# Performance work log

Hardware: AMD Instinct MI355X
Metric: run time of the kernel (lower is better)

The kernel has to match this reference:

```python
import jax, jax.numpy as jnp
import numpy as np

B, S, D, H, DH = 2, 2048, 1024, 16, 64
GLOBAL_RATIO = 0.1
LN_EPS = 1e-5


def setup_inputs() -> dict:
    key = jax.random.key(0)
    ks = jax.random.split(key, 8)
    w = lambda k, shape: jax.random.normal(k, shape, jnp.float32) * 0.02
    return {
        'x': jax.random.normal(ks[0], (B, S, D), jnp.float32),
        'Wq': w(ks[1], (D, H * DH)),
        'Wk': w(ks[2], (D, H * DH)),
        'Wv': w(ks[3], (D, H * DH)),
        'Wo': w(ks[4], (H * DH, D)),
        'bo': jnp.zeros((D,), jnp.float32),
        'ln_gamma': jnp.ones((DH,), jnp.float32),
        'ln_beta': jnp.zeros((DH,), jnp.float32),
        'Wg': w(ks[5], (2 * DH, DH)),
        'bg': jnp.zeros((DH,), jnp.float32),
    }


def _layernorm(x, gamma, beta):
    mu = jnp.mean(x, axis=-1, keepdims=True)
    var = jnp.mean(jnp.square(x - mu), axis=-1, keepdims=True)
    return (x - mu) * jax.lax.rsqrt(var + LN_EPS) * gamma + beta


def reference(x, Wq, Wk, Wv, Wo, bo, ln_gamma, ln_beta, Wg, bg):
    b, s, _ = x.shape
    # projections -> [b, h, n, d]
    split = lambda t: t.reshape(b, s, H, DH).transpose(0, 2, 1, 3)
    q = split(x @ Wq)
    k = split(x @ Wk)
    v = split(x @ Wv)
    scale = DH ** -0.5

    # local (full) attention: manual QK^T / softmax / AV
    scores = jnp.einsum('bhnd,bhmd->bhnm', q, k) * scale  # [b,h,s,s]
    attn = jax.nn.softmax(scores, axis=-1)
    local_out = jnp.einsum('bhnm,bhmd->bhnd', attn, v)

    # cross-segment fusion: top-k keys by norm per (b, h)
    num_global = max(1, int(s * GLOBAL_RATIO))
    key_norms = jnp.linalg.norm(k, axis=-1)  # [b,h,s]
    _, top_idx = jax.lax.top_k(key_norms, num_global)  # [b,h,g]
    idx = top_idx[..., None]  # [b,h,g,1]
    global_k = jnp.take_along_axis(k, idx, axis=2)  # [b,h,g,d]
    global_v = jnp.take_along_axis(v, idx, axis=2)
    g_scores = jnp.einsum('bhnd,bhgd->bhng', q, global_k) * scale
    g_attn = jax.nn.softmax(g_scores, axis=-1)
    global_out = jnp.einsum('bhng,bhgd->bhnd', g_attn, global_v)
    global_out = _layernorm(global_out, ln_gamma, ln_beta)

    # learned gate over [local, global]
    cat = jnp.concatenate([local_out, global_out], axis=-1)  # [b,h,s,2d]
    gate = jax.nn.sigmoid(cat @ Wg + bg)
    fused = gate * local_out + (1.0 - gate) * global_out

    out = fused.transpose(0, 2, 1, 3).reshape(b, s, H * DH)  # b h n d -> b n (h d)
    return out @ Wo + bo
```

## Files before the change

kernel.cpp:

```cpp
#include <hip/hip_runtime.h>


constexpr int SEQ    = 2048;
constexpr int DMODEL = 1024;
constexpr int NH     = 16;
constexpr int DHEAD  = 64;
constexpr int BHT    = 32;
constexpr int NG     = 204;
constexpr int NGPAD  = 256;
constexpr float LNEPS = 1e-5f;

typedef __attribute__((ext_vector_type(8))) short short8;
typedef __attribute__((ext_vector_type(4))) short short4v;
typedef __attribute__((ext_vector_type(4))) float f32x4;

__device__ __forceinline__ unsigned short f2bf(float f) {
    unsigned int u = __float_as_uint(f);
    u += 0x7FFFu + ((u >> 16) & 1u);
    return (unsigned short)(u >> 16);
}
__device__ __forceinline__ float bf2f(unsigned short b) {
    return __uint_as_float(((unsigned int)b) << 16);
}

__global__ __launch_bounds__(256)
void prep_k(const float* __restrict__ x,
            const float* __restrict__ Wq, const float* __restrict__ Wv,
            const float* __restrict__ Wo, const float* __restrict__ Wk,
            const float* __restrict__ Wg,
            unsigned short* __restrict__ xh, unsigned short* __restrict__ xl,
            unsigned short* __restrict__ Wqt, unsigned short* __restrict__ Wvt,
            unsigned short* __restrict__ Wot, unsigned short* __restrict__ Wkh,
            unsigned short* __restrict__ Wkl, unsigned short* __restrict__ Wgt)
{
    const int bid = blockIdx.x;
    const int tid = threadIdx.x;

    if (bid < 2048) {
        int i = (bid * 256 + tid) << 3;
        short8 h, l;
#pragma unroll
        for (int j = 0; j < 8; ++j) {
            float v = x[i + j];
            unsigned short hb = f2bf(v);
            h[j] = (short)hb;
            l[j] = (short)f2bf(v - bf2f(hb));
        }
        *(short8*)(xh + i) = h;
        *(short8*)(xl + i) = l;
        return;
    }
    if (bid == 3072) {
#pragma unroll
        for (int i = 0; i < 32; ++i) {
            int o = tid * 32 + i;
            int dg = o >> 7, jj = o & 127;
            Wgt[o] = f2bf(Wg[jj * 64 + dg]);
        }
        return;
    }

    __shared__ float tile[64][68];
    const int sub = bid - 2048;
    const int which = sub >> 8;
    const int b = sub & 255;
    const int n0 = (b & 15) * 64, k0 = (b >> 4) * 64;
    const float* W = (which == 0) ? Wq : (which == 1) ? Wv : (which == 2) ? Wo : Wk;
    const int Kd = DMODEL, Nd = DMODEL;

#pragma unroll
    for (int p = 0; p < 4; ++p) {
        int c = tid + (p << 8);
        int r = c >> 4, c4 = (c & 15) << 2;
        *(float4*)&tile[r][c4] = *(const float4*)(W + (size_t)(k0 + r) * Nd + n0 + c4);
    }
    __syncthreads();
#pragma unroll
    for (int p = 0; p < 4; ++p) {
        int c = tid + (p << 8);
        int n = c >> 4, k4 = (c & 15) << 2;
        if (which < 3) {
            unsigned short* Wt = (which == 0) ? Wqt : (which == 1) ? Wvt : Wot;
            short4v o;
#pragma unroll
            for (int j = 0; j < 4; ++j) o[j] = (short)f2bf(tile[k4 + j][n]);
            *(short4v*)(Wt + (size_t)(n0 + n) * Kd + k0 + k4) = o;
        } else {
            short4v oh, ol;
#pragma unroll
            for (int j = 0; j < 4; ++j) {
                float v = tile[k4 + j][n];
                unsigned short hb = f2bf(v);
                oh[j] = (short)hb;
                ol[j] = (short)f2bf(v - bf2f(hb));
            }
            *(short4v*)(Wkh + (size_t)(n0 + n) * Kd + k0 + k4) = oh;
            *(short4v*)(Wkl + (size_t)(n0 + n) * Kd + k0 + k4) = ol;
        }
    }
}

__global__ __launch_bounds__(512)
void gemm_bf16_k(const unsigned short* __restrict__ A,
                 const unsigned short* __restrict__ Bt,
                 const float* __restrict__ bias,
                 void* __restrict__ outv, void* __restrict__ outv2,
                 unsigned short* __restrict__ vtout,
                 int M, int N, int K, int mode)
{
    __shared__ __align__(16) unsigned short As[128][72];
    __shared__ __align__(16) unsigned short Bs[128][72];
    const int tid = threadIdx.x;
    const int lane = tid & 63, wave = tid >> 6;
    const int quad = lane >> 4, ln = lane & 15;
    const int mh = (wave >> 2) << 6;
    const int nh = (wave & 3) << 5;
    const int m0 = blockIdx.y * 128, n0 = blockIdx.x * 128;

    f32x4 acc[4][2];
#pragma unroll
    for (int i = 0; i < 4; ++i)
#pragma unroll
        for (int j = 0; j < 2; ++j) acc[i][j] = (f32x4){0.f, 0.f, 0.f, 0.f};

    short8 areg[2], breg[2];
#pragma unroll
    for (int p = 0; p < 2; ++p) {
        int c = tid + (p << 9);
        int row = c >> 3, col8 = (c & 7) << 3;
        areg[p] = *(const short8*)(A + (size_t)(m0 + row) * K + col8);
        breg[p] = *(const short8*)(Bt + (size_t)(n0 + row) * K + col8);
    }

    for (int k0 = 0; k0 < K; k0 += 64) {
        __syncthreads();
#pragma unroll
        for (int p = 0; p < 2; ++p) {
            int c = tid + (p << 9);
            int row = c >> 3, col8 = (c & 7) << 3;
            *(short8*)&As[row][col8] = areg[p];
            *(short8*)&Bs[row][col8] = breg[p];
        }
        __syncthreads();
        if (k0 + 64 < K) {
#pragma unroll
            for (int p = 0; p < 2; ++p) {
                int c = tid + (p << 9);
                int row = c >> 3, col8 = (c & 7) << 3;
                areg[p] = *(const short8*)(A + (size_t)(m0 + row) * K + k0 + 64 + col8);
                breg[p] = *(const short8*)(Bt + (size_t)(n0 + row) * K + k0 + 64 + col8);
            }
        }
#pragma unroll
        for (int ch = 0; ch < 2; ++ch) {
            short8 af[4], bf[2];
#pragma unroll
            for (int mt = 0; mt < 4; ++mt)
                af[mt] = *(const short8*)&As[mh + mt * 16 + ln][ch * 32 + quad * 8];
#pragma unroll
            for (int nt = 0; nt < 2; ++nt)
                bf[nt] = *(const short8*)&Bs[nh + nt * 16 + ln][ch * 32 + quad * 8];
#pragma unroll
            for (int mt = 0; mt < 4; ++mt)
#pragma unroll
                for (int nt = 0; nt < 2; ++nt)
                    acc[mt][nt] = __builtin_amdgcn_mfma_f32_16x16x32_bf16(
                        af[mt], bf[nt], acc[mt][nt], 0, 0, 0);
        }
    }

    if (mode == 0) {
        float* out = (float*)outv;
#pragma unroll
        for (int mt = 0; mt < 4; ++mt)
#pragma unroll
            for (int nt = 0; nt < 2; ++nt)
#pragma unroll
                for (int r = 0; r < 4; ++r) {
                    int m = m0 + mh + mt * 16 + quad * 4 + r;
                    int n = n0 + nh + nt * 16 + ln;
                    out[(size_t)m * N + n] = acc[mt][nt][r] + bias[n];
                }
    } else {
#pragma unroll
        for (int mt = 0; mt < 4; ++mt)
#pragma unroll
            for (int nt = 0; nt < 2; ++nt) {
                int n = n0 + nh + nt * 16 + ln;
                int mb = m0 + mh + mt * 16 + quad * 4;
                int b = mb >> 11, s0 = mb & (SEQ - 1);
                int d = n & 63;
                if (n < DMODEL) {
                    int h = n >> 6;
                    unsigned short* qp_ =
                        (unsigned short*)outv + ((size_t)(b * NH + h) * SEQ + s0) * DHEAD + d;
#pragma unroll
                    for (int r = 0; r < 4; ++r)
                        qp_[(size_t)r * DHEAD] = f2bf(acc[mt][nt][r] * 0.125f);
                } else {
                    int h = (n >> 6) - NH;
                    unsigned short* vp_ =
                        (unsigned short*)outv2 + ((size_t)(b * NH + h) * SEQ + s0) * DHEAD + d;
                    short4v tv;
#pragma unroll
                    for (int r = 0; r < 4; ++r) {
                        unsigned short bv = f2bf(acc[mt][nt][r]);
                        vp_[(size_t)r * DHEAD] = bv;
                        tv[r] = (short)bv;
                    }
                    *(short4v*)(vtout + ((size_t)(b * NH + h) * DHEAD + d) * SEQ + s0) = tv;
                }
            }
    }
}

__global__ __launch_bounds__(512)
void gemm_kproj_mfma(const unsigned short* __restrict__ xh,
                     const unsigned short* __restrict__ xl,
                     const unsigned short* __restrict__ Wh,
                     const unsigned short* __restrict__ Wl,
                     unsigned short* __restrict__ kout,
                     float* __restrict__ norms2)
{
    __shared__ __align__(16) unsigned short Ah[64][72];
    __shared__ __align__(16) unsigned short Al[64][72];
    __shared__ __align__(16) unsigned short Bh[128][72];
    __shared__ __align__(16) unsigned short Bl[128][72];
    const int K = DMODEL;
    const int tid = threadIdx.x;
    const int lane = tid & 63, wave = tid >> 6;
    const int quad = lane >> 4, ln = lane & 15;
    const int mh = (wave >> 1) << 4;
    const int nh = (wave & 1) << 6;
    const int m0 = blockIdx.y * 64, n0 = blockIdx.x * 128;

    f32x4 acc[4];
#pragma unroll
    for (int j = 0; j < 4; ++j) acc[j] = (f32x4){0.f, 0.f, 0.f, 0.f};

    const int arow = tid >> 3, acol8 = (tid & 7) << 3;
    short8 ahreg, alreg, bhreg[2], blreg[2];
    {
        size_t ga = (size_t)(m0 + arow) * K + acol8;
        ahreg = *(const short8*)(xh + ga);
        alreg = *(const short8*)(xl + ga);
#pragma unroll
        for (int p = 0; p < 2; ++p) {
            int c = tid + (p << 9);
            int row = c >> 3, col8 = (c & 7) << 3;
            size_t gb = (size_t)(n0 + row) * K + col8;
            bhreg[p] = *(const short8*)(Wh + gb);
            blreg[p] = *(const short8*)(Wl + gb);
        }
    }

    for (int k0 = 0; k0 < K; k0 += 64) {
        __syncthreads();
        *(short8*)&Ah[arow][acol8] = ahreg;
        *(short8*)&Al[arow][acol8] = alreg;
#pragma unroll
        for (int p = 0; p < 2; ++p) {
            int c = tid + (p << 9);
            int row = c >> 3, col8 = (c & 7) << 3;
            *(short8*)&Bh[row][col8] = bhreg[p];
            *(short8*)&Bl[row][col8] = blreg[p];
        }
        __syncthreads();
        if (k0 + 64 < K) {
            size_t ga = (size_t)(m0 + arow) * K + k0 + 64 + acol8;
            ahreg = *(const short8*)(xh + ga);
            alreg = *(const short8*)(xl + ga);
#pragma unroll
            for (int p = 0; p < 2; ++p) {
                int c = tid + (p << 9);
                int row = c >> 3, col8 = (c & 7) << 3;
                size_t gb = (size_t)(n0 + row) * K + k0 + 64 + col8;
                bhreg[p] = *(const short8*)(Wh + gb);
                blreg[p] = *(const short8*)(Wl + gb);
            }
        }
#pragma unroll
        for (int ch = 0; ch < 2; ++ch) {
            short8 bh4[4], bl4[4];
#pragma unroll
            for (int nt = 0; nt < 4; ++nt) {
                bh4[nt] = *(const short8*)&Bh[nh + nt * 16 + ln][ch * 32 + quad * 8];
                bl4[nt] = *(const short8*)&Bl[nh + nt * 16 + ln][ch * 32 + quad * 8];
            }
            short8 ah = *(const short8*)&Ah[mh + ln][ch * 32 + quad * 8];
            short8 al = *(const short8*)&Al[mh + ln][ch * 32 + quad * 8];
#pragma unroll
            for (int nt = 0; nt < 4; ++nt) {
                acc[nt] = __builtin_amdgcn_mfma_f32_16x16x32_bf16(ah, bh4[nt], acc[nt], 0, 0, 0);
                acc[nt] = __builtin_amdgcn_mfma_f32_16x16x32_bf16(ah, bl4[nt], acc[nt], 0, 0, 0);
                acc[nt] = __builtin_amdgcn_mfma_f32_16x16x32_bf16(al, bh4[nt], acc[nt], 0, 0, 0);
            }
        }
    }

    const int h = (n0 + nh) >> 6;
#pragma unroll
    for (int r = 0; r < 4; ++r) {
        int m = m0 + mh + quad * 4 + r;
        int b = m >> 11, s = m & (SEQ - 1);
        size_t rowbase = ((size_t)(b * NH + h) * SEQ + s) * DHEAD;
#pragma unroll
        for (int nt = 0; nt < 4; ++nt)
            kout[rowbase + nt * 16 + ln] = f2bf(acc[nt][r]);
        float s2 = acc[0][r] * acc[0][r] + acc[1][r] * acc[1][r] +
                   acc[2][r] * acc[2][r] + acc[3][r] * acc[3][r];
#pragma unroll
        for (int off = 1; off <= 8; off <<= 1)
            s2 += __shfl_xor(s2, off);
        if (ln == 0)
            norms2[(size_t)(b * NH + h) * SEQ + s] = s2;
    }
}

__global__ __launch_bounds__(512)
void topk_gather_k(const float* __restrict__ norms2,
                   const unsigned short* __restrict__ k,
                   const unsigned short* __restrict__ v,
                   unsigned short* __restrict__ gk,
                   unsigned short* __restrict__ gvt)
{
    __shared__ unsigned long long keys[SEQ];
    __shared__ int tix[NGPAD];
    __shared__ __align__(16) unsigned short T[64][72];
    const int bh = blockIdx.x;
    const int tid = threadIdx.x;
    const float* nb = norms2 + (size_t)bh * SEQ;
    const size_t base = (size_t)bh * SEQ * DHEAD;

    for (int i = tid; i < SEQ; i += 512) {
        float nrm = sqrtf(nb[i]);
        keys[i] = ((unsigned long long)__float_as_uint(nrm) << 32) |
                  (unsigned int)(0xFFFFFFFFu - (unsigned int)i);
    }
    __syncthreads();
    for (int kk = 2; kk <= SEQ; kk <<= 1) {
        for (int j = kk >> 1; j > 0; j >>= 1) {
            for (int i = tid; i < SEQ; i += 512) {
                int ixj = i ^ j;
                if (ixj > i) {
                    unsigned long long a = keys[i], b = keys[ixj];
                    bool up = ((i & kk) == 0);
                    if ((a > b) == up) { keys[i] = b; keys[ixj] = a; }
                }
            }
            __syncthreads();
        }
    }
    if (tid < NGPAD) {
        tix[tid] = (tid < NG)
            ? (int)(0xFFFFFFFFu - (unsigned int)(keys[SEQ - 1 - tid] & 0xFFFFFFFFu))
            : 0;
    }
    __syncthreads();

    for (int t = 0; t < NGPAD / 64; ++t) {
        {
            int idx = tid;
            int row = idx >> 3, col8 = (idx & 7) << 3;
            int g = t * 64 + row;
            short8 kv = (short8)0, vv = (short8)0;
            if (g < NG) {
                int sidx = tix[g];
                kv = *(const short8*)(k + base + (size_t)sidx * DHEAD + col8);
                vv = *(const short8*)(v + base + (size_t)sidx * DHEAD + col8);
            }
            *(short8*)(gk + ((size_t)bh * NGPAD + g) * DHEAD + col8) = kv;
            *(short8*)&T[row][col8] = vv;
        }
        __syncthreads();
        {
            int idx = tid;
            int d = idx >> 3, k8 = (idx & 7) << 3;
            short8 o;
#pragma unroll
            for (int i = 0; i < 8; ++i) o[i] = (short)T[k8 + i][d];
            *(short8*)(gvt + ((size_t)bh * DHEAD + d) * NGPAD + t * 64 + k8) = o;
        }
        __syncthreads();
    }
}

__global__ __launch_bounds__(512)
void attn_fused_k(const unsigned short* __restrict__ qb,
                  const unsigned short* __restrict__ kb,
                  const unsigned short* __restrict__ vt,
                  const unsigned short* __restrict__ gk,
                  const unsigned short* __restrict__ gvt,
                  const unsigned short* __restrict__ Wgt,
                  const float* __restrict__ gamma,
                  const float* __restrict__ beta,
                  const float* __restrict__ bg,
                  unsigned short* __restrict__ fused)
{
    __shared__ __align__(16) unsigned short Ks[64][72];
    __shared__ __align__(16) unsigned short Vt[64][72];
    __shared__ __align__(16) unsigned short Ps[128][72];
    __shared__ __align__(16) unsigned short Wgs[64][136];
    const int flat = blockIdx.x;
    const int bh = ((flat >> 7) << 3) | (flat & 7);
    const int q0 = ((flat >> 3) & 15) * 128;
    const int tid = threadIdx.x;
    const int lane = tid & 63, wave = tid >> 6;
    const int quad = lane >> 4, ln = lane & 15;
    const size_t base = (size_t)bh * SEQ * DHEAD;
    const unsigned short* gkb = gk + (size_t)bh * NGPAD * DHEAD;
    const unsigned short* gvb = gvt + (size_t)bh * DHEAD * NGPAD;

#pragma unroll
    for (int p = 0; p < 2; ++p) {
        int idx = tid + (p << 9);
        *(short8*)&Wgs[idx >> 4][(idx & 15) << 3] = *(const short8*)(Wgt + idx * 8);
    }

    short8 qf0, qf1;
    {
        const unsigned short* qp = qb + base + (size_t)(q0 + wave * 16 + ln) * DHEAD;
        qf0 = *(const short8*)(qp + quad * 8);
        qf1 = *(const short8*)(qp + 32 + quad * 8);
    }

    f32x4 O[4], Og[4];
#pragma unroll
    for (int nt = 0; nt < 4; ++nt) {
        O[nt] = (f32x4){0.f, 0.f, 0.f, 0.f};
        Og[nt] = (f32x4){0.f, 0.f, 0.f, 0.f};
    }
    float ls[4] = {0.f, 0.f, 0.f, 0.f};
    float lg[4] = {0.f, 0.f, 0.f, 0.f};

    short8 kreg = *(const short8*)(kb + base + (size_t)(tid >> 3) * DHEAD + ((tid & 7) << 3));
    short8 vreg = *(const short8*)(vt + base + (size_t)(tid >> 3) * SEQ + ((tid & 7) << 3));
    const int srow = tid >> 3, scol8 = (tid & 7) << 3;

    for (int t = 0; t < SEQ / 64; ++t) {
        __syncthreads();
        *(short8*)&Ks[srow][scol8] = kreg;
        *(short8*)&Vt[srow][scol8] = vreg;
        __syncthreads();
        if (t + 1 < SEQ / 64) {
            kreg = *(const short8*)(kb + base + (size_t)((t + 1) * 64 + srow) * DHEAD + scol8);
            vreg = *(const short8*)(vt + base + (size_t)srow * SEQ + (t + 1) * 64 + scol8);
        } else {
            kreg = *(const short8*)(gkb + (size_t)srow * DHEAD + scol8);
            vreg = *(const short8*)(gvb + (size_t)srow * NGPAD + scol8);
        }

        f32x4 s[4];
#pragma unroll
        for (int nt = 0; nt < 4; ++nt) {
            s[nt] = (f32x4){0.f, 0.f, 0.f, 0.f};
            short8 kf0 = *(const short8*)&Ks[nt * 16 + ln][quad * 8];
            short8 kf1 = *(const short8*)&Ks[nt * 16 + ln][32 + quad * 8];
            s[nt] = __builtin_amdgcn_mfma_f32_16x16x32_bf16(qf0, kf0, s[nt], 0, 0, 0);
            s[nt] = __builtin_amdgcn_mfma_f32_16x16x32_bf16(qf1, kf1, s[nt], 0, 0, 0);
        }
#pragma unroll
        for (int nt = 0; nt < 4; ++nt)
#pragma unroll
            for (int r = 0; r < 4; ++r) {
                float p = __expf(s[nt][r]);
                unsigned int us = __float_as_uint(p) >> 16;
                Ps[wave * 16 + quad * 4 + r][nt * 16 + ln] = (unsigned short)us;
                ls[r] += __uint_as_float(us << 16);
            }
#pragma unroll
        for (int ch = 0; ch < 2; ++ch) {
            short8 pf = *(const short8*)&Ps[wave * 16 + ln][ch * 32 + quad * 8];
#pragma unroll
            for (int nt = 0; nt < 4; ++nt) {
                short8 vf = *(const short8*)&Vt[nt * 16 + ln][ch * 32 + quad * 8];
                O[nt] = __builtin_amdgcn_mfma_f32_16x16x32_bf16(pf, vf, O[nt], 0, 0, 0);
            }
        }
    }

    for (int t = 0; t < NGPAD / 64; ++t) {
        __syncthreads();
        *(short8*)&Ks[srow][scol8] = kreg;
        *(short8*)&Vt[srow][scol8] = vreg;
        __syncthreads();
        if (t + 1 < NGPAD / 64) {
            kreg = *(const short8*)(gkb + (size_t)((t + 1) * 64 + srow) * DHEAD + scol8);
            vreg = *(const short8*)(gvb + (size_t)srow * NGPAD + (t + 1) * 64 + scol8);
        }

        f32x4 s[4];
#pragma unroll
        for (int nt = 0; nt < 4; ++nt) {
            s[nt] = (f32x4){0.f, 0.f, 0.f, 0.f};
            short8 kf0 = *(const short8*)&Ks[nt * 16 + ln][quad * 8];
            short8 kf1 = *(const short8*)&Ks[nt * 16 + ln][32 + quad * 8];
            s[nt] = __builtin_amdgcn_mfma_f32_16x16x32_bf16(qf0, kf0, s[nt], 0, 0, 0);
            s[nt] = __builtin_amdgcn_mfma_f32_16x16x32_bf16(qf1, kf1, s[nt], 0, 0, 0);
        }
#pragma unroll
        for (int nt = 0; nt < 4; ++nt) {
            bool valid = (t * 64 + nt * 16 + ln) < NG;
#pragma unroll
            for (int r = 0; r < 4; ++r) {
                float p = valid ? __expf(s[nt][r]) : 0.f;
                unsigned int us = __float_as_uint(p) >> 16;
                Ps[wave * 16 + quad * 4 + r][nt * 16 + ln] = (unsigned short)us;
                lg[r] += __uint_as_float(us << 16);
            }
        }
#pragma unroll
        for (int ch = 0; ch < 2; ++ch) {
            short8 pf = *(const short8*)&Ps[wave * 16 + ln][ch * 32 + quad * 8];
#pragma unroll
            for (int nt = 0; nt < 4; ++nt) {
                short8 vf = *(const short8*)&Vt[nt * 16 + ln][ch * 32 + quad * 8];
                Og[nt] = __builtin_amdgcn_mfma_f32_16x16x32_bf16(pf, vf, Og[nt], 0, 0, 0);
            }
        }
    }

#pragma unroll
    for (int off = 1; off <= 8; off <<= 1)
#pragma unroll
        for (int r = 0; r < 4; ++r) {
            ls[r] += __shfl_xor(ls[r], off);
            lg[r] += __shfl_xor(lg[r], off);
        }
    float invl[4];
#pragma unroll
    for (int r = 0; r < 4; ++r) invl[r] = 1.f / ls[r];

    float xs[4][4];
#pragma unroll
    for (int r = 0; r < 4; ++r) {
        float inv = 1.f / lg[r];
#pragma unroll
        for (int nt = 0; nt < 4; ++nt) xs[nt][r] = Og[nt][r] * inv;
    }
    float mu[4], rsd[4];
#pragma unroll
    for (int r = 0; r < 4; ++r) {
        float sm = xs[0][r] + xs[1][r] + xs[2][r] + xs[3][r];
#pragma unroll
        for (int off = 1; off <= 8; off <<= 1) sm += __shfl_xor(sm, off);
        mu[r] = sm * (1.f / 64.f);
    }
#pragma unroll
    for (int r = 0; r < 4; ++r) {
        float sv = 0.f;
#pragma unroll
        for (int nt = 0; nt < 4; ++nt) {
            float d = xs[nt][r] - mu[r];
            sv += d * d;
        }
#pragma unroll
        for (int off = 1; off <= 8; off <<= 1) sv += __shfl_xor(sv, off);
        rsd[r] = rsqrtf(sv * (1.f / 64.f) + LNEPS);
    }
#pragma unroll
    for (int nt = 0; nt < 4; ++nt) {
        float g = gamma[nt * 16 + ln], bb = beta[nt * 16 + ln];
#pragma unroll
        for (int r = 0; r < 4; ++r)
            xs[nt][r] = (xs[nt][r] - mu[r]) * rsd[r] * g + bb;
    }

    float lf[4][4];
#pragma unroll
    for (int nt = 0; nt < 4; ++nt)
#pragma unroll
        for (int r = 0; r < 4; ++r) {
            lf[nt][r] = O[nt][r] * invl[r];
            Ps[wave * 16 + quad * 4 + r][nt * 16 + ln] = f2bf(lf[nt][r]);
        }
    f32x4 gacc[4];
#pragma unroll
    for (int ng = 0; ng < 4; ++ng) {
        float bgv = bg[ng * 16 + ln];
        gacc[ng] = (f32x4){bgv, bgv, bgv, bgv};
    }
#pragma unroll
    for (int ch = 0; ch < 2; ++ch) {
        short8 af = *(const short8*)&Ps[wave * 16 + ln][ch * 32 + quad * 8];
#pragma unroll
        for (int ng = 0; ng < 4; ++ng) {
            short8 bf = *(const short8*)&Wgs[ng * 16 + ln][ch * 32 + quad * 8];
            gacc[ng] = __builtin_amdgcn_mfma_f32_16x16x32_bf16(af, bf, gacc[ng], 0, 0, 0);
        }
    }
#pragma unroll
    for (int nt = 0; nt < 4; ++nt)
#pragma unroll
        for (int r = 0; r < 4; ++r)
            Ps[wave * 16 + quad * 4 + r][nt * 16 + ln] = f2bf(xs[nt][r]);
#pragma unroll
    for (int ch = 0; ch < 2; ++ch) {
        short8 af = *(const short8*)&Ps[wave * 16 + ln][ch * 32 + quad * 8];
#pragma unroll
        for (int ng = 0; ng < 4; ++ng) {
            short8 bf = *(const short8*)&Wgs[ng * 16 + ln][64 + ch * 32 + quad * 8];
            gacc[ng] = __builtin_amdgcn_mfma_f32_16x16x32_bf16(af, bf, gacc[ng], 0, 0, 0);
        }
    }

    const int b = bh >> 4, h = bh & 15;
#pragma unroll
    for (int ng = 0; ng < 4; ++ng)
#pragma unroll
        for (int r = 0; r < 4; ++r) {
            float gt = 1.f / (1.f + __expf(-gacc[ng][r]));
            float f = gt * lf[ng][r] + (1.f - gt) * xs[ng][r];
            int s = q0 + wave * 16 + quad * 4 + r;
            fused[((size_t)(b * SEQ + s)) * DMODEL + h * DHEAD + ng * 16 + ln] = f2bf(f);
        }
}

extern "C" void kernel_launch(void* const* d_in, const int* in_sizes, int n_in,
                              void* d_out, int out_size, void* d_ws, size_t ws_size,
                              hipStream_t stream)
{
    (void)in_sizes; (void)n_in; (void)out_size; (void)ws_size;
    const float* x    = (const float*)d_in[0];
    const float* Wq   = (const float*)d_in[1];
    const float* Wk   = (const float*)d_in[2];
    const float* Wv   = (const float*)d_in[3];
    const float* Wo   = (const float*)d_in[4];
    const float* bo   = (const float*)d_in[5];
    const float* ln_g = (const float*)d_in[6];
    const float* ln_b = (const float*)d_in[7];
    const float* Wg   = (const float*)d_in[8];
    const float* bg   = (const float*)d_in[9];

    char* w = (char*)d_ws;
    const size_t MB = 1024ull * 1024ull;
    unsigned short* kb16  = (unsigned short*)(w);
    unsigned short* qb16  = (unsigned short*)(w + 8 * MB);
    unsigned short* vb16  = (unsigned short*)(w + 16 * MB);
    unsigned short* vt16  = (unsigned short*)(w + 24 * MB);
    unsigned short* xh    = (unsigned short*)(w + 32 * MB);
    unsigned short* xl    = (unsigned short*)(w + 40 * MB);
    unsigned short* Wqt   = (unsigned short*)(w + 48 * MB);
    unsigned short* Wvt   = (unsigned short*)(w + 50 * MB);
    unsigned short* Wot   = (unsigned short*)(w + 52 * MB);
    unsigned short* Wkh   = (unsigned short*)(w + 54 * MB);
    unsigned short* Wkl   = (unsigned short*)(w + 56 * MB);
    unsigned short* Wgt   = (unsigned short*)(w + 58 * MB);
    float*          norms2= (float*)(w + 59 * MB);
    unsigned short* gk16  = (unsigned short*)(w + 60 * MB);
    unsigned short* gvt16 = (unsigned short*)(w + 61 * MB);
    unsigned short* fusedb = xh;

    const int M = 4096, N = 1024, K = 1024;

    prep_k<<<3073, 256, 0, stream>>>(x, Wq, Wv, Wo, Wk, Wg,
                                     xh, xl, Wqt, Wvt, Wot, Wkh, Wkl, Wgt);

    dim3 gqv(2048 / 128, M / 128);
    gemm_bf16_k<<<gqv, 512, 0, stream>>>(xh, Wqt, nullptr, qb16, vb16, vt16,
                                         M, 2048, K, 3);

    dim3 gkp(N / 128, M / 64);
    gemm_kproj_mfma<<<gkp, 512, 0, stream>>>(xh, xl, Wkh, Wkl, kb16, norms2);

    topk_gather_k<<<BHT, 512, 0, stream>>>(norms2, kb16, vb16, gk16, gvt16);

    attn_fused_k<<<512, 512, 0, stream>>>(qb16, kb16, vt16, gk16, gvt16, Wgt,
                                          ln_g, ln_b, bg, fusedb);

    dim3 go_(N / 128, M / 128);
    gemm_bf16_k<<<go_, 512, 0, stream>>>(fusedb, Wot, bo, (float*)d_out, nullptr,
                                         nullptr, M, N, K, 0);
}
```

Measured before the change: 301.7 us.

## Give each attention wave two query tiles and halve the block size

The fused attention kernel now runs 256 threads (4 waves) per block instead of 512, and each wave handles 32 query rows as two 16-row MFMA tiles. Each K and V fragment read from LDS is therefore reused for two MFMAs, which halves LDS fragment traffic per MFMA and gives fewer waves per block taking part in each barrier. s_setprio is also raised around the MFMA sections to favour matrix issue across waves. The cost is roughly double the accumulator registers per wave, which can lower occupancy even with launch_bounds(256,2), and the global-to-LDS staging loads per thread double.

```diff
diff --git a/kernel.cpp b/kernel.cpp
--- a/kernel.cpp
+++ b/kernel.cpp
@@ -385,7 +385,7 @@
     }
 }
 
-__global__ __launch_bounds__(512)
+__global__ __launch_bounds__(256, 2)
 void attn_fused_k(const unsigned short* __restrict__ qb,
                   const unsigned short* __restrict__ kb,
                   const unsigned short* __restrict__ vt,
@@ -412,208 +412,300 @@
     const unsigned short* gvb = gvt + (size_t)bh * DHEAD * NGPAD;
 
 #pragma unroll
+    for (int p = 0; p < 4; ++p) {
+        int idx = tid + (p << 8);
+        *(short8*)&Wgs[idx >> 4][(idx & 15) << 3] = *(const short8*)(Wgt + idx * 8);
+    }
+
+    short8 qf[2][2];
+#pragma unroll
+    for (int mt = 0; mt < 2; ++mt) {
+        const unsigned short* qp = qb + base + (size_t)(q0 + wave * 32 + mt * 16 + ln) * DHEAD;
+        qf[mt][0] = *(const short8*)(qp + quad * 8);
+        qf[mt][1] = *(const short8*)(qp + 32 + quad * 8);
+    }
+
+    f32x4 O[2][4], Og[2][4];
+#pragma unroll
+    for (int mt = 0; mt < 2; ++mt)
+#pragma unroll
+        for (int nt = 0; nt < 4; ++nt) {
+            O[mt][nt] = (f32x4){0.f, 0.f, 0.f, 0.f};
+            Og[mt][nt] = (f32x4){0.f, 0.f, 0.f, 0.f};
+        }
+    float ls[2][4], lg[2][4];
+#pragma unroll
+    for (int mt = 0; mt < 2; ++mt)
+#pragma unroll
+        for (int r = 0; r < 4; ++r) { ls[mt][r] = 0.f; lg[mt][r] = 0.f; }
+
+    short8 kreg[2], vreg[2];
+    int srow[2], scol8[2];
+#pragma unroll
     for (int p = 0; p < 2; ++p) {
-        int idx = tid + (p << 9);
-        *(short8*)&Wgs[idx >> 4][(idx & 15) << 3] = *(const short8*)(Wgt + idx * 8);
-    }
-
-    short8 qf0, qf1;
-    {
-        const unsigned short* qp = qb + base + (size_t)(q0 + wave * 16 + ln) * DHEAD;
-        qf0 = *(const short8*)(qp + quad * 8);
-        qf1 = *(const short8*)(qp + 32 + quad * 8);
-    }
-
-    f32x4 O[4], Og[4];
-#pragma unroll
-    for (int nt = 0; nt < 4; ++nt) {
-        O[nt] = (f32x4){0.f, 0.f, 0.f, 0.f};
-        Og[nt] = (f32x4){0.f, 0.f, 0.f, 0.f};
-    }
-    float ls[4] = {0.f, 0.f, 0.f, 0.f};
-    float lg[4] = {0.f, 0.f, 0.f, 0.f};
-
-    short8 kreg = *(const short8*)(kb + base + (size_t)(tid >> 3) * DHEAD + ((tid & 7) << 3));
-    short8 vreg = *(const short8*)(vt + base + (size_t)(tid >> 3) * SEQ + ((tid & 7) << 3));
-    const int srow = tid >> 3, scol8 = (tid & 7) << 3;
+        int idx = tid + (p << 8);
+        srow[p] = idx >> 3;
+        scol8[p] = (idx & 7) << 3;
+        kreg[p] = *(const short8*)(kb + base + (size_t)srow[p] * DHEAD + scol8[p]);
+        vreg[p] = *(const short8*)(vt + base + (size_t)srow[p] * SEQ + scol8[p]);
+    }
 
     for (int t = 0; t < SEQ / 64; ++t) {
         __syncthreads();
-        *(short8*)&Ks[srow][scol8] = kreg;
-        *(short8*)&Vt[srow][scol8] = vreg;
+#pragma unroll
+        for (int p = 0; p < 2; ++p) {
+            *(short8*)&Ks[srow[p]][scol8[p]] = kreg[p];
+            *(short8*)&Vt[srow[p]][scol8[p]] = vreg[p];
+        }
         __syncthreads();
         if (t + 1 < SEQ / 64) {
-            kreg = *(const short8*)(kb + base + (size_t)((t + 1) * 64 + srow) * DHEAD + scol8);
-            vreg = *(const short8*)(vt + base + (size_t)srow * SEQ + (t + 1) * 64 + scol8);
+#pragma unroll
+            for (int p = 0; p < 2; ++p) {
+                kreg[p] = *(const short8*)(kb + base + (size_t)((t + 1) * 64 + srow[p]) * DHEAD + scol8[p]);
+                vreg[p] = *(const short8*)(vt + base + (size_t)srow[p] * SEQ + (t + 1) * 64 + scol8[p]);
+            }
         } else {
-            kreg = *(const short8*)(gkb + (size_t)srow * DHEAD + scol8);
-            vreg = *(const short8*)(gvb + (size_t)srow * NGPAD + scol8);
-        }
-
-        f32x4 s[4];
+#pragma unroll
+            for (int p = 0; p < 2; ++p) {
+                kreg[p] = *(const short8*)(gkb + (size_t)srow[p] * DHEAD + scol8[p]);
+                vreg[p] = *(const short8*)(gvb + (size_t)srow[p] * NGPAD + scol8[p]);
+            }
+        }
+
+        f32x4 s[2][4];
+#pragma unroll
+        for (int mt = 0; mt < 2; ++mt)
+#pragma unroll
+            for (int nt = 0; nt < 4; ++nt) s[mt][nt] = (f32x4){0.f, 0.f, 0.f, 0.f};
+        __builtin_amdgcn_s_setprio(1);
 #pragma unroll
         for (int nt = 0; nt < 4; ++nt) {
-            s[nt] = (f32x4){0.f, 0.f, 0.f, 0.f};
             short8 kf0 = *(const short8*)&Ks[nt * 16 + ln][quad * 8];
             short8 kf1 = *(const short8*)&Ks[nt * 16 + ln][32 + quad * 8];
-            s[nt] = __builtin_amdgcn_mfma_f32_16x16x32_bf16(qf0, kf0, s[nt], 0, 0, 0);
-            s[nt] = __builtin_amdgcn_mfma_f32_16x16x32_bf16(qf1, kf1, s[nt], 0, 0, 0);
-        }
-#pragma unroll
-        for (int nt = 0; nt < 4; ++nt)
-#pragma unroll
-            for (int r = 0; r < 4; ++r) {
-                float p = __expf(s[nt][r]);
-                unsigned int us = __float_as_uint(p) >> 16;
-                Ps[wave * 16 + quad * 4 + r][nt * 16 + ln] = (unsigned short)us;
-                ls[r] += __uint_as_float(us << 16);
-            }
+#pragma unroll
+            for (int mt = 0; mt < 2; ++mt) {
+                s[mt][nt] = __builtin_amdgcn_mfma_f32_16x16x32_bf16(qf[mt][0], kf0, s[mt][nt], 0, 0, 0);
+                s[mt][nt] = __builtin_amdgcn_mfma_f32_16x16x32_bf16(qf[mt][1], kf1, s[mt][nt], 0, 0, 0);
+            }
+        }
+        __builtin_amdgcn_s_setprio(0);
+#pragma unroll
+        for (int mt = 0; mt < 2; ++mt)
+#pragma unroll
+            for (int nt = 0; nt < 4; ++nt)
+#pragma unroll
+                for (int r = 0; r < 4; ++r) {
+                    float p = __expf(s[mt][nt][r]);
+                    unsigned int us = __float_as_uint(p) >> 16;
+                    Ps[wave * 32 + mt * 16 + quad * 4 + r][nt * 16 + ln] = (unsigned short)us;
+                    ls[mt][r] += __uint_as_float(us << 16);
+                }
 #pragma unroll
         for (int ch = 0; ch < 2; ++ch) {
-            short8 pf = *(const short8*)&Ps[wave * 16 + ln][ch * 32 + quad * 8];
+            short8 pf[2];
+#pragma unroll
+            for (int mt = 0; mt < 2; ++mt)
+                pf[mt] = *(const short8*)&Ps[wave * 32 + mt * 16 + ln][ch * 32 + quad * 8];
+            __builtin_amdgcn_s_setprio(1);
 #pragma unroll
             for (int nt = 0; nt < 4; ++nt) {
                 short8 vf = *(const short8*)&Vt[nt * 16 + ln][ch * 32 + quad * 8];
-                O[nt] = __builtin_amdgcn_mfma_f32_16x16x32_bf16(pf, vf, O[nt], 0, 0, 0);
-            }
+#pragma unroll
+                for (int mt = 0; mt < 2; ++mt)
+                    O[mt][nt] = __builtin_amdgcn_mfma_f32_16x16x32_bf16(pf[mt], vf, O[mt][nt], 0, 0, 0);
+            }
+            __builtin_amdgcn_s_setprio(0);
         }
     }
 
     for (int t = 0; t < NGPAD / 64; ++t) {
         __syncthreads();
-        *(short8*)&Ks[srow][scol8] = kreg;
-        *(short8*)&Vt[srow][scol8] = vreg;
+#pragma unroll
+        for (int p = 0; p < 2; ++p) {
+            *(short8*)&Ks[srow[p]][scol8[p]] = kreg[p];
+            *(short8*)&Vt[srow[p]][scol8[p]] = vreg[p];
+        }
         __syncthreads();
         if (t + 1 < NGPAD / 64) {
-            kreg = *(const short8*)(gkb + (size_t)((t + 1) * 64 + srow) * DHEAD + scol8);
-            vreg = *(const short8*)(gvb + (size_t)srow * NGPAD + (t + 1) * 64 + scol8);
-        }
-
-        f32x4 s[4];
+#pragma unroll
+            for (int p = 0; p < 2; ++p) {
+                kreg[p] = *(const short8*)(gkb + (size_t)((t + 1) * 64 + srow[p]) * DHEAD + scol8[p]);
+                vreg[p] = *(const short8*)(gvb + (size_t)srow[p] * NGPAD + (t + 1) * 64 + scol8[p]);
+            }
+        }
+
+        f32x4 s[2][4];
+#pragma unroll
+        for (int mt = 0; mt < 2; ++mt)
+#pragma unroll
+            for (int nt = 0; nt < 4; ++nt) s[mt][nt] = (f32x4){0.f, 0.f, 0.f, 0.f};
+        __builtin_amdgcn_s_setprio(1);
 #pragma unroll
         for (int nt = 0; nt < 4; ++nt) {
-            s[nt] = (f32x4){0.f, 0.f, 0.f, 0.f};
             short8 kf0 = *(const short8*)&Ks[nt * 16 + ln][quad * 8];
             short8 kf1 = *(const short8*)&Ks[nt * 16 + ln][32 + quad * 8];
-            s[nt] = __builtin_amdgcn_mfma_f32_16x16x32_bf16(qf0, kf0, s[nt], 0, 0, 0);
-            s[nt] = __builtin_amdgcn_mfma_f32_16x16x32_bf16(qf1, kf1, s[nt], 0, 0, 0);
-        }
+#pragma unroll
+            for (int mt = 0; mt < 2; ++mt) {
+                s[mt][nt] = __builtin_amdgcn_mfma_f32_16x16x32_bf16(qf[mt][0], kf0, s[mt][nt], 0, 0, 0);
+                s[mt][nt] = __builtin_amdgcn_mfma_f32_16x16x32_bf16(qf[mt][1], kf1, s[mt][nt], 0, 0, 0);
+            }
+        }
+        __builtin_amdgcn_s_setprio(0);
 #pragma unroll
         for (int nt = 0; nt < 4; ++nt) {
             bool valid = (t * 64 + nt * 16 + ln) < NG;
 #pragma unroll
-            for (int r = 0; r < 4; ++r) {
-                float p = valid ? __expf(s[nt][r]) : 0.f;
-                unsigned int us = __float_as_uint(p) >> 16;
-                Ps[wave * 16 + quad * 4 + r][nt * 16 + ln] = (unsigned short)us;
-                lg[r] += __uint_as_float(us << 16);
-            }
+            for (int mt = 0; mt < 2; ++mt)
+#pragma unroll
+                for (int r = 0; r < 4; ++r) {
+                    float p = valid ? __expf(s[mt][nt][r]) : 0.f;
+                    unsigned int us = __float_as_uint(p) >> 16;
+                    Ps[wave * 32 + mt * 16 + quad * 4 + r][nt * 16 + ln] = (unsigned short)us;
+                    lg[mt][r] += __uint_as_float(us << 16);
+                }
         }
 #pragma unroll
         for (int ch = 0; ch < 2; ++ch) {
-            short8 pf = *(const short8*)&Ps[wave * 16 + ln][ch * 32 + quad * 8];
+            short8 pf[2];
+#pragma unroll
+            for (int mt = 0; mt < 2; ++mt)
+                pf[mt] = *(const short8*)&Ps[wave * 32 + mt * 16 + ln][ch * 32 + quad * 8];
+            __builtin_amdgcn_s_setprio(1);
 #pragma unroll
             for (int nt = 0; nt < 4; ++nt) {
                 short8 vf = *(const short8*)&Vt[nt * 16 + ln][ch * 32 + quad * 8];
-                Og[nt] = __builtin_amdgcn_mfma_f32_16x16x32_bf16(pf, vf, Og[nt], 0, 0, 0);
-            }
+#pragma unroll
+                for (int mt = 0; mt < 2; ++mt)
+                    Og[mt][nt] = __builtin_amdgcn_mfma_f32_16x16x32_bf16(pf[mt], vf, Og[mt][nt], 0, 0, 0);
+            }
+            __builtin_amdgcn_s_setprio(0);
         }
     }
 
 #pragma unroll
     for (int off = 1; off <= 8; off <<= 1)
 #pragma unroll
+        for (int mt = 0; mt < 2; ++mt)
+#pragma unroll
+            for (int r = 0; r < 4; ++r) {
+                ls[mt][r] += __shfl_xor(ls[mt][r], off);
+                lg[mt][r] += __shfl_xor(lg[mt][r], off);
+            }
+    float invl[2][4];
+#pragma unroll
+    for (int mt = 0; mt < 2; ++mt)
+#pragma unroll
+        for (int r = 0; r < 4; ++r) invl[mt][r] = 1.f / ls[mt][r];
+
+    float xs[2][4][4];
+#pragma unroll
+    for (int mt = 0; mt < 2; ++mt)
+#pragma unroll
         for (int r = 0; r < 4; ++r) {
-            ls[r] += __shfl_xor(ls[r], off);
-            lg[r] += __shfl_xor(lg[r], off);
-        }
-    float invl[4];
-#pragma unroll
-    for (int r = 0; r < 4; ++r) invl[r] = 1.f / ls[r];
-
-    float xs[4][4];
-#pragma unroll
-    for (int r = 0; r < 4; ++r) {
-        float inv = 1.f / lg[r];
-#pragma unroll
-        for (int nt = 0; nt < 4; ++nt) xs[nt][r] = Og[nt][r] * inv;
-    }
-    float mu[4], rsd[4];
-#pragma unroll
-    for (int r = 0; r < 4; ++r) {
-        float sm = xs[0][r] + xs[1][r] + xs[2][r] + xs[3][r];
-#pragma unroll
-        for (int off = 1; off <= 8; off <<= 1) sm += __shfl_xor(sm, off);
-        mu[r] = sm * (1.f / 64.f);
-    }
-#pragma unroll
-    for (int r = 0; r < 4; ++r) {
-        float sv = 0.f;
-#pragma unroll
-        for (int nt = 0; nt < 4; ++nt) {
-            float d = xs[nt][r] - mu[r];
-            sv += d * d;
-        }
-#pragma unroll
-        for (int off = 1; off <= 8; off <<= 1) sv += __shfl_xor(sv, off);
-        rsd[r] = rsqrtf(sv * (1.f / 64.f) + LNEPS);
-    }
+            float inv = 1.f / lg[mt][r];
+#pragma unroll
+            for (int nt = 0; nt < 4; ++nt) xs[mt][nt][r] = Og[mt][nt][r] * inv;
+        }
+    float mu[2][4], rsd[2][4];
+#pragma unroll
+    for (int mt = 0; mt < 2; ++mt)
+#pragma unroll
+        for (int r = 0; r < 4; ++r) {
+            float sm = xs[mt][0][r] + xs[mt][1][r] + xs[mt][2][r] + xs[mt][3][r];
+#pragma unroll
+            for (int off = 1; off <= 8; off <<= 1) sm += __shfl_xor(sm, off);
+            mu[mt][r] = sm * (1.f / 64.f);
+        }
+#pragma unroll
+    for (int mt = 0; mt < 2; ++mt)
+#pragma unroll
+        for (int r = 0; r < 4; ++r) {
+            float sv = 0.f;
+#pragma unroll
+            for (int nt = 0; nt < 4; ++nt) {
+                float d = xs[mt][nt][r] - mu[mt][r];
+                sv += d * d;
+            }
+#pragma unroll
+            for (int off = 1; off <= 8; off <<= 1) sv += __shfl_xor(sv, off);
+            rsd[mt][r] = rsqrtf(sv * (1.f / 64.f) + LNEPS);
+        }
 #pragma unroll
     for (int nt = 0; nt < 4; ++nt) {
         float g = gamma[nt * 16 + ln], bb = beta[nt * 16 + ln];
 #pragma unroll
-        for (int r = 0; r < 4; ++r)
-            xs[nt][r] = (xs[nt][r] - mu[r]) * rsd[r] * g + bb;
-    }
-
-    float lf[4][4];
-#pragma unroll
-    for (int nt = 0; nt < 4; ++nt)
-#pragma unroll
-        for (int r = 0; r < 4; ++r) {
-            lf[nt][r] = O[nt][r] * invl[r];
-            Ps[wave * 16 + quad * 4 + r][nt * 16 + ln] = f2bf(lf[nt][r]);
-        }
-    f32x4 gacc[4];
+        for (int mt = 0; mt < 2; ++mt)
+#pragma unroll
+            for (int r = 0; r < 4; ++r)
+                xs[mt][nt][r] = (xs[mt][nt][r] - mu[mt][r]) * rsd[mt][r] * g + bb;
+    }
+
+    float lf[2][4][4];
+#pragma unroll
+    for (int mt = 0; mt < 2; ++mt)
+#pragma unroll
+        for (int nt = 0; nt < 4; ++nt)
+#pragma unroll
+            for (int r = 0; r < 4; ++r) {
+                lf[mt][nt][r] = O[mt][nt][r] * invl[mt][r];
+                Ps[wave * 32 + mt * 16 + quad * 4 + r][nt * 16 + ln] = f2bf(lf[mt][nt][r]);
+            }
+    f32x4 gacc[2][4];
 #pragma unroll
     for (int ng = 0; ng < 4; ++ng) {
         float bgv = bg[ng * 16 + ln];
-        gacc[ng] = (f32x4){bgv, bgv, bgv, bgv};
+#pragma unroll
+        for (int mt = 0; mt < 2; ++mt)
+            gacc[mt][ng] = (f32x4){bgv, bgv, bgv, bgv};
     }
 #pragma unroll
     for (int ch = 0; ch < 2; ++ch) {
-        short8 af = *(const short8*)&Ps[wave * 16 + ln][ch * 32 + quad * 8];
+        short8 af[2];
+#pragma unroll
+        for (int mt = 0; mt < 2; ++mt)
+            af[mt] = *(const short8*)&Ps[wave * 32 + mt * 16 + ln][ch * 32 + quad * 8];
 #pragma unroll
         for (int ng = 0; ng < 4; ++ng) {
             short8 bf = *(const short8*)&Wgs[ng * 16 + ln][ch * 32 + quad * 8];
-            gacc[ng] = __builtin_amdgcn_mfma_f32_16x16x32_bf16(af, bf, gacc[ng], 0, 0, 0);
-        }
-    }
-#pragma unroll
-    for (int nt = 0; nt < 4; ++nt)
-#pragma unroll
-        for (int r = 0; r < 4; ++r)
-            Ps[wave * 16 + quad * 4 + r][nt * 16 + ln] = f2bf(xs[nt][r]);
+#pragma unroll
+            for (int mt = 0; mt < 2; ++mt)
+                gacc[mt][ng] = __builtin_amdgcn_mfma_f32_16x16x32_bf16(af[mt], bf, gacc[mt][ng], 0, 0, 0);
+        }
+    }
+#pragma unroll
+    for (int mt = 0; mt < 2; ++mt)
+#pragma unroll
+        for (int nt = 0; nt < 4; ++nt)
+#pragma unroll
+            for (int r = 0; r < 4; ++r)
+                Ps[wave * 32 + mt * 16 + quad * 4 + r][nt * 16 + ln] = f2bf(xs[mt][nt][r]);
 #pragma unroll
     for (int ch = 0; ch < 2; ++ch) {
-        short8 af = *(const short8*)&Ps[wave * 16 + ln][ch * 32 + quad * 8];
+        short8 af[2];
+#pragma unroll
+        for (int mt = 0; mt < 2; ++mt)
+            af[mt] = *(const short8*)&Ps[wave * 32 + mt * 16 + ln][ch * 32 + quad * 8];
 #pragma unroll
         for (int ng = 0; ng < 4; ++ng) {
             short8 bf = *(const short8*)&Wgs[ng * 16 + ln][64 + ch * 32 + quad * 8];
-            gacc[ng] = __builtin_amdgcn_mfma_f32_16x16x32_bf16(af, bf, gacc[ng], 0, 0, 0);
+#pragma unroll
+            for (int mt = 0; mt < 2; ++mt)
+                gacc[mt][ng] = __builtin_amdgcn_mfma_f32_16x16x32_bf16(af[mt], bf, gacc[mt][ng], 0, 0, 0);
         }
     }
 
     const int b = bh >> 4, h = bh & 15;
 #pragma unroll
-    for (int ng = 0; ng < 4; ++ng)
-#pragma unroll
-        for (int r = 0; r < 4; ++r) {
-            float gt = 1.f / (1.f + __expf(-gacc[ng][r]));
-            float f = gt * lf[ng][r] + (1.f - gt) * xs[ng][r];
-            int s = q0 + wave * 16 + quad * 4 + r;
-            fused[((size_t)(b * SEQ + s)) * DMODEL + h * DHEAD + ng * 16 + ln] = f2bf(f);
-        }
+    for (int mt = 0; mt < 2; ++mt)
+#pragma unroll
+        for (int ng = 0; ng < 4; ++ng)
+#pragma unroll
+            for (int r = 0; r < 4; ++r) {
+                float gt = 1.f / (1.f + __expf(-gacc[mt][ng][r]));
+                float f = gt * lf[mt][ng][r] + (1.f - gt) * xs[mt][ng][r];
+                int s = q0 + wave * 32 + mt * 16 + quad * 4 + r;
+                fused[((size_t)(b * SEQ + s)) * DMODEL + h * DHEAD + ng * 16 + ln] = f2bf(f);
+            }
 }
 
 extern "C" void kernel_launch(void* const* d_in, const int* in_sizes, int n_in,
@@ -665,7 +757,7 @@
 
     topk_gather_k<<<BHT, 512, 0, stream>>>(norms2, kb16, vb16, gk16, gvt16);
 
-    attn_fused_k<<<512, 512, 0, stream>>>(qb16, kb16, vt16, gk16, gvt16, Wgt,
+    attn_fused_k<<<512, 256, 0, stream>>>(qb16, kb16, vt16, gk16, gvt16, Wgt,
                                           ln_g, ln_b, bg, fusedb);
 
     dim3 go_(N / 128, M / 128);
```

Result: faster. 284.4 us (-5.7%).
